# Kernel tuning notes

Measured on AMD Instinct MI355X. Metric: run time of the kernel, lower is better.

Reference implementation:

```python
import jax, jax.numpy as jnp
import numpy as np

N, C_IN, C_RED, H, W = 16, 256, 64, 48, 48


def conv1x1(x, w, b):
    # x: [N, Cin, H, W], w: [Cout, Cin], b: [Cout]
    return jnp.einsum('nchw,oc->nohw', x, w) + b[None, :, None, None]


def setup_inputs() -> dict:
    key = jax.random.key(0)
    ks = jax.random.split(key, 10)
    s_in = 1.0 / np.sqrt(C_IN)
    s_red = 1.0 / np.sqrt(C_RED)
    return {
        'feature_maps': jax.random.normal(ks[0], (N, C_IN, H, W), jnp.float32),
        'global_channel_output': jax.random.normal(ks[1], (N, C_IN, H, W), jnp.float32),
        'Wq': jax.random.uniform(ks[2], (C_RED, C_IN), jnp.float32, -s_in, s_in),
        'bq': jax.random.uniform(ks[3], (C_RED,), jnp.float32, -s_in, s_in),
        'Wk': jax.random.uniform(ks[4], (C_RED, C_IN), jnp.float32, -s_in, s_in),
        'bk': jax.random.uniform(ks[5], (C_RED,), jnp.float32, -s_in, s_in),
        'Wv': jax.random.uniform(ks[6], (C_RED, C_IN), jnp.float32, -s_in, s_in),
        'bv': jax.random.uniform(ks[7], (C_RED,), jnp.float32, -s_in, s_in),
        'Watt': jax.random.uniform(ks[8], (C_IN, C_RED), jnp.float32, -s_red, s_red),
        'batt': jax.random.uniform(ks[9], (C_IN,), jnp.float32, -s_red, s_red),
    }


def reference(feature_maps, global_channel_output, Wq, bq, Wk, bk, Wv, bv, Watt, batt):
    n, _, h, w = feature_maps.shape
    hw = h * w
    q = conv1x1(feature_maps, Wq, bq).reshape(n, -1, hw)   # [N, Cr, HW]
    k = conv1x1(feature_maps, Wk, bk).reshape(n, -1, hw)   # [N, Cr, HW]
    v = conv1x1(feature_maps, Wv, bv).reshape(n, -1, hw)   # [N, Cr, HW]
    # key^T @ query -> [N, HW, HW]
    qk = jnp.einsum('nci,ncj->nij', k, q)
    # global (flattened) softmax over the whole HWxHW matrix per batch element
    qk = jax.nn.softmax(qk.reshape(n, hw * hw), axis=-1).reshape(n, hw, hw)
    att = jnp.einsum('nci,nij->ncj', v, qk).reshape(n, -1, h, w)  # [N, Cr, H, W]
    att = conv1x1(att, Watt, batt)                                 # [N, Cin, H, W]
    return global_channel_output * att + global_channel_output
```

## Files before the change

kernel.cpp:

```cpp
#include <hip/hip_runtime.h>
#include <hip/hip_bf16.h>
#include <stdint.h>

#define NB   16
#define CIN  256
#define CRED 64
#define HW   2304
#define NJT_OUT 36
#define JT_ATT  128
#define NJT_ATT 18
#define NIG  4
#define NIT  9

typedef __bf16 bf16;
typedef __bf16 bf16x8 __attribute__((ext_vector_type(8)));
typedef __bf16 bf16x4 __attribute__((ext_vector_type(4)));
typedef float  f32x4  __attribute__((ext_vector_type(4)));

__global__ __launch_bounds__(256) void prep_kernel(
    const float* __restrict__ Wq, const float* __restrict__ bq,
    const float* __restrict__ Wk, const float* __restrict__ Wv,
    const float* __restrict__ Watt,
    bf16* __restrict__ Wqb, bf16* __restrict__ Wkb, bf16* __restrict__ Wvb,
    bf16* __restrict__ Wab, float* __restrict__ bqs)
{
    const float INVLN2 = 1.44269504088896f;
    int i = blockIdx.x * 256 + threadIdx.x;
    Wqb[i] = (bf16)(Wq[i] * INVLN2);
    Wkb[i] = (bf16)Wk[i];
    Wvb[i] = (bf16)Wv[i];
    Wab[i] = (bf16)Watt[i];
    if (i < CRED) bqs[i] = bq[i] * INVLN2;
}

__global__ __launch_bounds__(256) void qkv_kernel(
    const float* __restrict__ x,
    const bf16* __restrict__ Wqb, const float* __restrict__ bqs,
    const bf16* __restrict__ Wkb, const float* __restrict__ bk,
    const bf16* __restrict__ Wvb, const float* __restrict__ bv,
    bf16* __restrict__ qT, bf16* __restrict__ kT, bf16* __restrict__ v)
{
    __shared__ __align__(16) bf16 sX[32 * 264];
    const int jt = blockIdx.x, n = blockIdx.y;
    const int jbase = jt * 32;
    const int tid = threadIdx.x;
    const int lane = tid & 63, w = tid >> 6;
    const int l15 = lane & 15, q4 = lane >> 4;

    const float* xn = x + ((size_t)n * CIN) * HW + jbase;
    #pragma unroll
    for (int it = 0; it < 8; ++it) {
        int idx = tid + 256 * it;
        int c = idx >> 3, p4 = idx & 7;
        const float4 vv = *(const float4*)(xn + c * HW + p4 * 4);
        sX[(p4 * 4 + 0) * 264 + c] = (bf16)vv.x;
        sX[(p4 * 4 + 1) * 264 + c] = (bf16)vv.y;
        sX[(p4 * 4 + 2) * 264 + c] = (bf16)vv.z;
        sX[(p4 * 4 + 3) * 264 + c] = (bf16)vv.w;
    }
    __syncthreads();

    const bf16*  Ws[3] = {Wqb, Wkb, Wvb};
    const float* bs[3] = {bqs, bk, bv};
    #pragma unroll
    for (int wi = 0; wi < 3; ++wi) {
        bf16x8 a[8];
        const bf16* Wp = Ws[wi] + (w * 16 + l15) * CIN + q4 * 8;
        #pragma unroll
        for (int ks = 0; ks < 8; ++ks) a[ks] = *(const bf16x8*)(Wp + ks * 32);
        f32x4 acc[2] = {};
        #pragma unroll
        for (int nt = 0; nt < 2; ++nt) {
            #pragma unroll
            for (int ks = 0; ks < 8; ++ks) {
                bf16x8 b = *(const bf16x8*)(sX + (nt * 16 + l15) * 264 + ks * 32 + q4 * 8);
                acc[nt] = __builtin_amdgcn_mfma_f32_16x16x32_bf16(a[ks], b, acc[nt], 0, 0, 0);
            }
        }
        const int crb = w * 16 + q4 * 4;
        const float b0 = bs[wi][crb], b1 = bs[wi][crb + 1],
                    b2 = bs[wi][crb + 2], b3 = bs[wi][crb + 3];
        if (wi < 2) {
            bf16* dst = (wi == 0 ? qT : kT) + ((size_t)n * HW) * 64;
            #pragma unroll
            for (int nt = 0; nt < 2; ++nt) {
                int pos = jbase + nt * 16 + l15;
                bf16x4 pk = {(bf16)(acc[nt].x + b0), (bf16)(acc[nt].y + b1),
                             (bf16)(acc[nt].z + b2), (bf16)(acc[nt].w + b3)};
                *(bf16x4*)(dst + pos * 64 + crb) = pk;
            }
        } else {
            bf16* dst = v + ((size_t)n * CRED) * HW;
            #pragma unroll
            for (int nt = 0; nt < 2; ++nt) {
                int pos = jbase + nt * 16 + l15;
                dst[(crb + 0) * HW + pos] = (bf16)(acc[nt].x + b0);
                dst[(crb + 1) * HW + pos] = (bf16)(acc[nt].y + b1);
                dst[(crb + 2) * HW + pos] = (bf16)(acc[nt].z + b2);
                dst[(crb + 3) * HW + pos] = (bf16)(acc[nt].w + b3);
            }
        }
    }
}

__global__ __launch_bounds__(256, 4) void attn_kernel(
    const bf16* __restrict__ qT, const bf16* __restrict__ kT,
    const bf16* __restrict__ v,
    float* __restrict__ OTp, float* __restrict__ Z)
{
    __shared__ __align__(16) bf16 sK[64 * 72];
    __shared__ __align__(16) bf16 sV[64 * 72];
    __shared__ __align__(16) bf16 sP[128 * 72];
    const int jt = blockIdx.x, ig = blockIdx.y, n = blockIdx.z;
    const int jbase = jt * JT_ATT;
    const int tid = threadIdx.x;
    const int lane = tid & 63, w = tid >> 6;
    const int l15 = lane & 15, q4 = lane >> 4;

    bf16x8 qf[2][2];
    {
        const bf16* qn = qT + ((size_t)n * HW + jbase + w * 32) * 64;
        #pragma unroll
        for (int nt = 0; nt < 2; ++nt)
            #pragma unroll
            for (int ks = 0; ks < 2; ++ks)
                qf[nt][ks] = *(const bf16x8*)(qn + (nt * 16 + l15) * 64 + ks * 32 + q4 * 8);
    }

    f32x4 oacc[4][2] = {};
    float zacc = 0.f;
    const uint4* ksrc = (const uint4*)(kT + ((size_t)n * HW) * 64);
    const bf16* vbase = v + ((size_t)n * CRED) * HW;

    const int r0 = tid >> 3, c0 = tid & 7;
    const int ibase0 = ig * NIT * 64;

    uint4 kr0 = ksrc[(ibase0 + r0) * 8 + c0];
    uint4 kr1 = ksrc[(ibase0 + r0 + 32) * 8 + c0];
    uint4 vr0 = *(const uint4*)(vbase + (size_t)r0 * HW + ibase0 + c0 * 8);
    uint4 vr1 = *(const uint4*)(vbase + (size_t)(r0 + 32) * HW + ibase0 + c0 * 8);

    uint4* dk = (uint4*)sK;
    uint4* dv = (uint4*)sV;
    bf16* sPw = sP + (w * 32) * 72;

    for (int it = 0; it < NIT; ++it) {
        __syncthreads();
        dk[r0 * 9 + c0] = kr0;
        dk[(r0 + 32) * 9 + c0] = kr1;
        dv[r0 * 9 + c0] = vr0;
        dv[(r0 + 32) * 9 + c0] = vr1;
        const int nbase = ibase0 + ((it + 1 < NIT) ? (it + 1) * 64 : 0);
        kr0 = ksrc[(nbase + r0) * 8 + c0];
        kr1 = ksrc[(nbase + r0 + 32) * 8 + c0];
        vr0 = *(const uint4*)(vbase + (size_t)r0 * HW + nbase + c0 * 8);
        vr1 = *(const uint4*)(vbase + (size_t)(r0 + 32) * HW + nbase + c0 * 8);
        __syncthreads();

        #pragma unroll
        for (int is = 0; is < 4; ++is) {
            bf16x8 kf0 = *(const bf16x8*)(sK + (is * 16 + l15) * 72 + q4 * 8);
            bf16x8 kf1 = *(const bf16x8*)(sK + (is * 16 + l15) * 72 + 32 + q4 * 8);
            #pragma unroll
            for (int nt = 0; nt < 2; ++nt) {
                f32x4 accs = {};
                accs = __builtin_amdgcn_mfma_f32_16x16x32_bf16(kf0, qf[nt][0], accs, 0, 0, 0);
                accs = __builtin_amdgcn_mfma_f32_16x16x32_bf16(kf1, qf[nt][1], accs, 0, 0, 0);
                float p0 = exp2f(accs.x), p1 = exp2f(accs.y);
                float p2 = exp2f(accs.z), p3 = exp2f(accs.w);
                zacc += (p0 + p1) + (p2 + p3);
                bf16x4 pk = {(bf16)p0, (bf16)p1, (bf16)p2, (bf16)p3};
                *(bf16x4*)(sPw + (nt * 16 + l15) * 72 + is * 16 + q4 * 4) = pk;
            }
        }
        bf16x8 pb[2][2];
        #pragma unroll
        for (int nt = 0; nt < 2; ++nt) {
            pb[nt][0] = *(const bf16x8*)(sPw + (nt * 16 + l15) * 72 + q4 * 8);
            pb[nt][1] = *(const bf16x8*)(sPw + (nt * 16 + l15) * 72 + 32 + q4 * 8);
        }
        #pragma unroll
        for (int ct = 0; ct < 4; ++ct) {
            bf16x8 vf0 = *(const bf16x8*)(sV + (ct * 16 + l15) * 72 + q4 * 8);
            bf16x8 vf1 = *(const bf16x8*)(sV + (ct * 16 + l15) * 72 + 32 + q4 * 8);
            #pragma unroll
            for (int nt = 0; nt < 2; ++nt) {
                oacc[ct][nt] = __builtin_amdgcn_mfma_f32_16x16x32_bf16(vf0, pb[nt][0], oacc[ct][nt], 0, 0, 0);
                oacc[ct][nt] = __builtin_amdgcn_mfma_f32_16x16x32_bf16(vf1, pb[nt][1], oacc[ct][nt], 0, 0, 0);
            }
        }
    }
    float* OTn = OTp + (((size_t)ig * NB + n) * HW) * 64;
    #pragma unroll
    for (int ct = 0; ct < 4; ++ct)
        #pragma unroll
        for (int nt = 0; nt < 2; ++nt) {
            int pos = jbase + w * 32 + nt * 16 + l15;
            *(f32x4*)(OTn + (size_t)pos * 64 + ct * 16 + q4 * 4) = oacc[ct][nt];
        }
    #pragma unroll
    for (int off = 32; off > 0; off >>= 1) zacc += __shfl_down(zacc, off);
    if (lane == 0) atomicAdd(Z + n, zacc);
}

__global__ __launch_bounds__(256) void out_kernel(
    const float* __restrict__ OTp, const float* __restrict__ Z,
    const bf16* __restrict__ Wab, const float* __restrict__ batt,
    const float* __restrict__ g, float* __restrict__ out)
{
    __shared__ __align__(16) bf16 sO[64 * 72];
    const int jt = blockIdx.x, n = blockIdx.y;
    const int jbase = jt * 64;
    const int tid = threadIdx.x;
    const int lane = tid & 63, w = tid >> 6;
    const int l15 = lane & 15, q4 = lane >> 4;
    const float invZ = 1.0f / Z[n];

    for (int i = tid; i < 1024; i += 256) {
        int r = i >> 4, c4 = i & 15;
        const float* p = OTp + (((size_t)n * HW) + jbase + r) * 64 + c4 * 4;
        float4 s = *(const float4*)(p);
        #pragma unroll
        for (int igx = 1; igx < NIG; ++igx) {
            float4 t = *(const float4*)(p + (size_t)igx * NB * HW * 64);
            s.x += t.x; s.y += t.y; s.z += t.z; s.w += t.w;
        }
        bf16x4 pk = {(bf16)(s.x * invZ), (bf16)(s.y * invZ),
                     (bf16)(s.z * invZ), (bf16)(s.w * invZ)};
        *(bf16x4*)(sO + r * 72 + c4 * 4) = pk;
    }
    __syncthreads();

    bf16x8 bfr[4][2];
    #pragma unroll
    for (int nt = 0; nt < 4; ++nt)
        #pragma unroll
        for (int ks = 0; ks < 2; ++ks)
            bfr[nt][ks] = *(const bf16x8*)(sO + (nt * 16 + l15) * 72 + ks * 32 + q4 * 8);

    const float* gp = g + ((size_t)n * CIN) * HW;
    float* op = out + ((size_t)n * CIN) * HW;
    #pragma unroll
    for (int mt = 0; mt < 4; ++mt) {
        const bf16* Wp = Wab + (w * 64 + mt * 16 + l15) * 64 + q4 * 8;
        bf16x8 a0 = *(const bf16x8*)(Wp);
        bf16x8 a1 = *(const bf16x8*)(Wp + 32);
        const int co = w * 64 + mt * 16 + q4 * 4;
        const float c0 = batt[co], c1 = batt[co + 1], c2 = batt[co + 2], c3 = batt[co + 3];
        #pragma unroll
        for (int nt = 0; nt < 4; ++nt) {
            f32x4 acc = {};
            acc = __builtin_amdgcn_mfma_f32_16x16x32_bf16(a0, bfr[nt][0], acc, 0, 0, 0);
            acc = __builtin_amdgcn_mfma_f32_16x16x32_bf16(a1, bfr[nt][1], acc, 0, 0, 0);
            const int pos = jbase + nt * 16 + l15;
            const float g0 = gp[(co + 0) * HW + pos], g1 = gp[(co + 1) * HW + pos];
            const float g2 = gp[(co + 2) * HW + pos], g3 = gp[(co + 3) * HW + pos];
            op[(co + 0) * HW + pos] = g0 * (acc.x + c0 + 1.0f);
            op[(co + 1) * HW + pos] = g1 * (acc.y + c1 + 1.0f);
            op[(co + 2) * HW + pos] = g2 * (acc.z + c2 + 1.0f);
            op[(co + 3) * HW + pos] = g3 * (acc.w + c3 + 1.0f);
        }
    }
}

extern "C" void kernel_launch(void* const* d_in, const int* in_sizes, int n_in,
                              void* d_out, int out_size, void* d_ws, size_t ws_size,
                              hipStream_t stream) {
    const float* x    = (const float*)d_in[0];
    const float* g    = (const float*)d_in[1];
    const float* Wq   = (const float*)d_in[2];
    const float* bq   = (const float*)d_in[3];
    const float* Wk   = (const float*)d_in[4];
    const float* bk   = (const float*)d_in[5];
    const float* Wv   = (const float*)d_in[6];
    const float* bv   = (const float*)d_in[7];
    const float* Watt = (const float*)d_in[8];
    const float* batt = (const float*)d_in[9];
    float* out = (float*)d_out;

    char* ws = (char*)d_ws;
    const size_t qkv_sz = (size_t)NB * HW * CRED * sizeof(bf16);
    bf16*  qT  = (bf16*)(ws);
    bf16*  kT  = (bf16*)(ws + qkv_sz);
    bf16*  vv  = (bf16*)(ws + 2 * qkv_sz);
    float* OTp = (float*)(ws + 3 * qkv_sz);
    char*  w2  = ws + 3 * qkv_sz + (size_t)NIG * NB * HW * CRED * sizeof(float);
    float* Zp  = (float*)(w2);
    bf16*  Wqb = (bf16*)(w2 + 256);
    bf16*  Wkb = Wqb + CRED * CIN;
    bf16*  Wvb = Wkb + CRED * CIN;
    bf16*  Wab = Wvb + CRED * CIN;
    float* bqs = (float*)(Wab + CIN * CRED);

    hipMemsetAsync(Zp, 0, NB * sizeof(float), stream);

    dim3 blk(256);
    prep_kernel<<<dim3(64), blk, 0, stream>>>(Wq, bq, Wk, Wv, Watt, Wqb, Wkb, Wvb, Wab, bqs);
    qkv_kernel<<<dim3(HW / 32, NB), blk, 0, stream>>>(x, Wqb, bqs, Wkb, bk, Wvb, bv, qT, kT, vv);
    attn_kernel<<<dim3(NJT_ATT, NIG, NB), blk, 0, stream>>>(qT, kT, vv, OTp, Zp);
    out_kernel<<<dim3(NJT_OUT, NB), blk, 0, stream>>>(OTp, Zp, Wab, batt, g, out);
}
```

Measured before the change: 248.7 us.

## Keep P in registers, split x transpose into own kernel, shrink out tiles

Several changes land together. The attention kernel no longer round-trips the softmax probabilities through shared memory; they are packed to bf16 with v_cvt_pk_bf16_f32, and a lane shuffle (xor 32) lines up the MFMA B-operand, with the V tile stored in shared memory in a permuted order to match. The QKV projection is split into a separate transpose-to-bf16 kernel, whose output reuses the OTp workspace, and an MFMA kernel that reads the transposed x directly from global memory and computes all three projections in one K loop. The output kernel tile is halved to 32 positions to launch more blocks. The extra launch and extra global traffic for xT add cost, and the permuted V layout adds correctness risk.

```diff
diff --git a/kernel.cpp b/kernel.cpp
--- a/kernel.cpp
+++ b/kernel.cpp
@@ -6,7 +6,6 @@
 #define CIN  256
 #define CRED 64
 #define HW   2304
-#define NJT_OUT 36
 #define JT_ATT  128
 #define NJT_ATT 18
 #define NIG  4
@@ -15,6 +14,7 @@
 typedef __bf16 bf16;
 typedef __bf16 bf16x8 __attribute__((ext_vector_type(8)));
 typedef __bf16 bf16x4 __attribute__((ext_vector_type(4)));
+typedef __bf16 bf16x2 __attribute__((ext_vector_type(2)));
 typedef float  f32x4  __attribute__((ext_vector_type(4)));
 
 __global__ __launch_bounds__(256) void prep_kernel(
@@ -33,72 +33,102 @@
     if (i < CRED) bqs[i] = bq[i] * INVLN2;
 }
 
-__global__ __launch_bounds__(256) void qkv_kernel(
-    const float* __restrict__ x,
+__global__ __launch_bounds__(256) void xpose_kernel(
+    const float* __restrict__ x, bf16* __restrict__ xT)
+{
+    __shared__ bf16 sT[64 * 74];
+    const int pt = blockIdx.x, ct = blockIdx.y, n = blockIdx.z;
+    const int tid = threadIdx.x;
+    const float* xb = x + ((size_t)n * CIN + ct * 64) * HW + pt * 64;
+    #pragma unroll
+    for (int i = 0; i < 4; ++i) {
+        int idx = tid + 256 * i;
+        int c = idx >> 4, p4 = idx & 15;
+        float4 vv = *(const float4*)(xb + (size_t)c * HW + p4 * 4);
+        bf16x2 e0 = {(bf16)vv.x, (bf16)vv.y};
+        bf16x2 e1 = {(bf16)vv.z, (bf16)vv.w};
+        *(bf16x2*)(sT + c * 74 + p4 * 4)     = e0;
+        *(bf16x2*)(sT + c * 74 + p4 * 4 + 2) = e1;
+    }
+    __syncthreads();
+    bf16* xo = xT + ((size_t)n * HW + pt * 64) * 256 + ct * 64;
+    #pragma unroll
+    for (int i = 0; i < 2; ++i) {
+        int idx = tid + 256 * i;
+        int pos = idx >> 3, c8 = (idx & 7) * 8;
+        bf16x8 o;
+        #pragma unroll
+        for (int e = 0; e < 8; ++e) o[e] = sT[(c8 + e) * 74 + pos];
+        *(bf16x8*)(xo + (size_t)pos * 256 + c8) = o;
+    }
+}
+
+__global__ __launch_bounds__(256) void qkvc_kernel(
+    const bf16* __restrict__ xT,
     const bf16* __restrict__ Wqb, const float* __restrict__ bqs,
     const bf16* __restrict__ Wkb, const float* __restrict__ bk,
     const bf16* __restrict__ Wvb, const float* __restrict__ bv,
     bf16* __restrict__ qT, bf16* __restrict__ kT, bf16* __restrict__ v)
 {
-    __shared__ __align__(16) bf16 sX[32 * 264];
     const int jt = blockIdx.x, n = blockIdx.y;
     const int jbase = jt * 32;
     const int tid = threadIdx.x;
     const int lane = tid & 63, w = tid >> 6;
     const int l15 = lane & 15, q4 = lane >> 4;
 
-    const float* xn = x + ((size_t)n * CIN) * HW + jbase;
-    #pragma unroll
-    for (int it = 0; it < 8; ++it) {
-        int idx = tid + 256 * it;
-        int c = idx >> 3, p4 = idx & 7;
-        const float4 vv = *(const float4*)(xn + c * HW + p4 * 4);
-        sX[(p4 * 4 + 0) * 264 + c] = (bf16)vv.x;
-        sX[(p4 * 4 + 1) * 264 + c] = (bf16)vv.y;
-        sX[(p4 * 4 + 2) * 264 + c] = (bf16)vv.z;
-        sX[(p4 * 4 + 3) * 264 + c] = (bf16)vv.w;
-    }
-    __syncthreads();
-
-    const bf16*  Ws[3] = {Wqb, Wkb, Wvb};
-    const float* bs[3] = {bqs, bk, bv};
-    #pragma unroll
-    for (int wi = 0; wi < 3; ++wi) {
-        bf16x8 a[8];
-        const bf16* Wp = Ws[wi] + (w * 16 + l15) * CIN + q4 * 8;
-        #pragma unroll
-        for (int ks = 0; ks < 8; ++ks) a[ks] = *(const bf16x8*)(Wp + ks * 32);
-        f32x4 acc[2] = {};
-        #pragma unroll
-        for (int nt = 0; nt < 2; ++nt) {
-            #pragma unroll
-            for (int ks = 0; ks < 8; ++ks) {
-                bf16x8 b = *(const bf16x8*)(sX + (nt * 16 + l15) * 264 + ks * 32 + q4 * 8);
-                acc[nt] = __builtin_amdgcn_mfma_f32_16x16x32_bf16(a[ks], b, acc[nt], 0, 0, 0);
-            }
-        }
-        const int crb = w * 16 + q4 * 4;
-        const float b0 = bs[wi][crb], b1 = bs[wi][crb + 1],
-                    b2 = bs[wi][crb + 2], b3 = bs[wi][crb + 3];
-        if (wi < 2) {
-            bf16* dst = (wi == 0 ? qT : kT) + ((size_t)n * HW) * 64;
-            #pragma unroll
-            for (int nt = 0; nt < 2; ++nt) {
-                int pos = jbase + nt * 16 + l15;
-                bf16x4 pk = {(bf16)(acc[nt].x + b0), (bf16)(acc[nt].y + b1),
-                             (bf16)(acc[nt].z + b2), (bf16)(acc[nt].w + b3)};
-                *(bf16x4*)(dst + pos * 64 + crb) = pk;
-            }
-        } else {
-            bf16* dst = v + ((size_t)n * CRED) * HW;
-            #pragma unroll
-            for (int nt = 0; nt < 2; ++nt) {
-                int pos = jbase + nt * 16 + l15;
-                dst[(crb + 0) * HW + pos] = (bf16)(acc[nt].x + b0);
-                dst[(crb + 1) * HW + pos] = (bf16)(acc[nt].y + b1);
-                dst[(crb + 2) * HW + pos] = (bf16)(acc[nt].z + b2);
-                dst[(crb + 3) * HW + pos] = (bf16)(acc[nt].w + b3);
-            }
+    const bf16* xb = xT + ((size_t)n * HW + jbase) * 256 + q4 * 8;
+    const bf16* W0 = Wqb + (size_t)(w * 16 + l15) * CIN + q4 * 8;
+    const bf16* W1 = Wkb + (size_t)(w * 16 + l15) * CIN + q4 * 8;
+    const bf16* W2 = Wvb + (size_t)(w * 16 + l15) * CIN + q4 * 8;
+
+    f32x4 acc[3][2] = {};
+    #pragma unroll
+    for (int ks = 0; ks < 8; ++ks) {
+        bf16x8 b0 = *(const bf16x8*)(xb + (size_t)l15 * 256 + ks * 32);
+        bf16x8 b1 = *(const bf16x8*)(xb + (size_t)(16 + l15) * 256 + ks * 32);
+        bf16x8 aq = *(const bf16x8*)(W0 + ks * 32);
+        bf16x8 ak = *(const bf16x8*)(W1 + ks * 32);
+        bf16x8 av = *(const bf16x8*)(W2 + ks * 32);
+        acc[0][0] = __builtin_amdgcn_mfma_f32_16x16x32_bf16(aq, b0, acc[0][0], 0, 0, 0);
+        acc[0][1] = __builtin_amdgcn_mfma_f32_16x16x32_bf16(aq, b1, acc[0][1], 0, 0, 0);
+        acc[1][0] = __builtin_amdgcn_mfma_f32_16x16x32_bf16(ak, b0, acc[1][0], 0, 0, 0);
+        acc[1][1] = __builtin_amdgcn_mfma_f32_16x16x32_bf16(ak, b1, acc[1][1], 0, 0, 0);
+        acc[2][0] = __builtin_amdgcn_mfma_f32_16x16x32_bf16(av, b0, acc[2][0], 0, 0, 0);
+        acc[2][1] = __builtin_amdgcn_mfma_f32_16x16x32_bf16(av, b1, acc[2][1], 0, 0, 0);
+    }
+    const int crb = w * 16 + q4 * 4;
+    {
+        const float b0 = bqs[crb], b1 = bqs[crb+1], b2 = bqs[crb+2], b3 = bqs[crb+3];
+        bf16* dst = qT + ((size_t)n * HW) * 64;
+        #pragma unroll
+        for (int nt = 0; nt < 2; ++nt) {
+            int pos = jbase + nt * 16 + l15;
+            bf16x4 pk = {(bf16)(acc[0][nt].x + b0), (bf16)(acc[0][nt].y + b1),
+                         (bf16)(acc[0][nt].z + b2), (bf16)(acc[0][nt].w + b3)};
+            *(bf16x4*)(dst + (size_t)pos * 64 + crb) = pk;
+        }
+    }
+    {
+        const float b0 = bk[crb], b1 = bk[crb+1], b2 = bk[crb+2], b3 = bk[crb+3];
+        bf16* dst = kT + ((size_t)n * HW) * 64;
+        #pragma unroll
+        for (int nt = 0; nt < 2; ++nt) {
+            int pos = jbase + nt * 16 + l15;
+            bf16x4 pk = {(bf16)(acc[1][nt].x + b0), (bf16)(acc[1][nt].y + b1),
+                         (bf16)(acc[1][nt].z + b2), (bf16)(acc[1][nt].w + b3)};
+            *(bf16x4*)(dst + (size_t)pos * 64 + crb) = pk;
+        }
+    }
+    {
+        const float b0 = bv[crb], b1 = bv[crb+1], b2 = bv[crb+2], b3 = bv[crb+3];
+        bf16* dst = v + ((size_t)n * CRED) * HW;
+        #pragma unroll
+        for (int nt = 0; nt < 2; ++nt) {
+            int pos = jbase + nt * 16 + l15;
+            dst[(crb + 0) * HW + pos] = (bf16)(acc[2][nt].x + b0);
+            dst[(crb + 1) * HW + pos] = (bf16)(acc[2][nt].y + b1);
+            dst[(crb + 2) * HW + pos] = (bf16)(acc[2][nt].z + b2);
+            dst[(crb + 3) * HW + pos] = (bf16)(acc[2][nt].w + b3);
         }
     }
 }
@@ -110,7 +140,6 @@
 {
     __shared__ __align__(16) bf16 sK[64 * 72];
     __shared__ __align__(16) bf16 sV[64 * 72];
-    __shared__ __align__(16) bf16 sP[128 * 72];
     const int jt = blockIdx.x, ig = blockIdx.y, n = blockIdx.z;
     const int jbase = jt * JT_ATT;
     const int tid = threadIdx.x;
@@ -135,58 +164,74 @@
     const int r0 = tid >> 3, c0 = tid & 7;
     const int ibase0 = ig * NIT * 64;
 
+    const int gg = c0 >> 2, m = c0 & 3;
+    const int kbA = ((m >> 1) & 1) | (((m ^ (m >> 1)) & 1) << 2);
+    bf16* vdst0 = sV + r0 * 72 + gg * 32 + kbA * 4;
+    bf16* vdst1 = sV + (r0 + 32) * 72 + gg * 32 + kbA * 4;
+
     uint4 kr0 = ksrc[(ibase0 + r0) * 8 + c0];
     uint4 kr1 = ksrc[(ibase0 + r0 + 32) * 8 + c0];
     uint4 vr0 = *(const uint4*)(vbase + (size_t)r0 * HW + ibase0 + c0 * 8);
     uint4 vr1 = *(const uint4*)(vbase + (size_t)(r0 + 32) * HW + ibase0 + c0 * 8);
 
     uint4* dk = (uint4*)sK;
-    uint4* dv = (uint4*)sV;
-    bf16* sPw = sP + (w * 32) * 72;
 
     for (int it = 0; it < NIT; ++it) {
         __syncthreads();
         dk[r0 * 9 + c0] = kr0;
         dk[(r0 + 32) * 9 + c0] = kr1;
-        dv[r0 * 9 + c0] = vr0;
-        dv[(r0 + 32) * 9 + c0] = vr1;
-        const int nbase = ibase0 + ((it + 1 < NIT) ? (it + 1) * 64 : 0);
+        {
+            uint2 lo, hi;
+            lo.x = vr0.x; lo.y = vr0.y; hi.x = vr0.z; hi.y = vr0.w;
+            *(uint2*)(vdst0) = lo; *(uint2*)(vdst0 + 8) = hi;
+            lo.x = vr1.x; lo.y = vr1.y; hi.x = vr1.z; hi.y = vr1.w;
+            *(uint2*)(vdst1) = lo; *(uint2*)(vdst1 + 8) = hi;
+        }
+        const int ibase = ibase0 + it * 64;
+        const int nbase = (it + 1 < NIT) ? ibase + 64 : ibase0;
         kr0 = ksrc[(nbase + r0) * 8 + c0];
         kr1 = ksrc[(nbase + r0 + 32) * 8 + c0];
         vr0 = *(const uint4*)(vbase + (size_t)r0 * HW + nbase + c0 * 8);
         vr1 = *(const uint4*)(vbase + (size_t)(r0 + 32) * HW + nbase + c0 * 8);
         __syncthreads();
 
+        unsigned pw[2][4][2];
         #pragma unroll
         for (int is = 0; is < 4; ++is) {
             bf16x8 kf0 = *(const bf16x8*)(sK + (is * 16 + l15) * 72 + q4 * 8);
             bf16x8 kf1 = *(const bf16x8*)(sK + (is * 16 + l15) * 72 + 32 + q4 * 8);
             #pragma unroll
             for (int nt = 0; nt < 2; ++nt) {
-                f32x4 accs = {};
-                accs = __builtin_amdgcn_mfma_f32_16x16x32_bf16(kf0, qf[nt][0], accs, 0, 0, 0);
-                accs = __builtin_amdgcn_mfma_f32_16x16x32_bf16(kf1, qf[nt][1], accs, 0, 0, 0);
-                float p0 = exp2f(accs.x), p1 = exp2f(accs.y);
-                float p2 = exp2f(accs.z), p3 = exp2f(accs.w);
+                f32x4 s = {};
+                s = __builtin_amdgcn_mfma_f32_16x16x32_bf16(kf0, qf[nt][0], s, 0, 0, 0);
+                s = __builtin_amdgcn_mfma_f32_16x16x32_bf16(kf1, qf[nt][1], s, 0, 0, 0);
+                float p0 = exp2f(s.x), p1 = exp2f(s.y);
+                float p2 = exp2f(s.z), p3 = exp2f(s.w);
                 zacc += (p0 + p1) + (p2 + p3);
-                bf16x4 pk = {(bf16)p0, (bf16)p1, (bf16)p2, (bf16)p3};
-                *(bf16x4*)(sPw + (nt * 16 + l15) * 72 + is * 16 + q4 * 4) = pk;
+                unsigned w0, w1;
+                asm("v_cvt_pk_bf16_f32 %0, %1, %2" : "=v"(w0) : "v"(p0), "v"(p1));
+                asm("v_cvt_pk_bf16_f32 %0, %1, %2" : "=v"(w1) : "v"(p2), "v"(p3));
+                pw[nt][is][0] = w0;
+                pw[nt][is][1] = w1;
             }
         }
-        bf16x8 pb[2][2];
-        #pragma unroll
-        for (int nt = 0; nt < 2; ++nt) {
-            pb[nt][0] = *(const bf16x8*)(sPw + (nt * 16 + l15) * 72 + q4 * 8);
-            pb[nt][1] = *(const bf16x8*)(sPw + (nt * 16 + l15) * 72 + 32 + q4 * 8);
-        }
-        #pragma unroll
-        for (int ct = 0; ct < 4; ++ct) {
-            bf16x8 vf0 = *(const bf16x8*)(sV + (ct * 16 + l15) * 72 + q4 * 8);
-            bf16x8 vf1 = *(const bf16x8*)(sV + (ct * 16 + l15) * 72 + 32 + q4 * 8);
+        #pragma unroll
+        for (int g = 0; g < 2; ++g) {
+            bf16x8 vf[4];
+            #pragma unroll
+            for (int ct = 0; ct < 4; ++ct)
+                vf[ct] = *(const bf16x8*)(sV + (ct * 16 + l15) * 72 + g * 32 + q4 * 8);
             #pragma unroll
             for (int nt = 0; nt < 2; ++nt) {
-                oacc[ct][nt] = __builtin_amdgcn_mfma_f32_16x16x32_bf16(vf0, pb[nt][0], oacc[ct][nt], 0, 0, 0);
-                oacc[ct][nt] = __builtin_amdgcn_mfma_f32_16x16x32_bf16(vf1, pb[nt][1], oacc[ct][nt], 0, 0, 0);
+                union { unsigned u[4]; bf16x8 v8; } pb;
+                pb.u[0] = pw[nt][2 * g][0];
+                pb.u[1] = pw[nt][2 * g][1];
+                pb.u[2] = (unsigned)__shfl_xor((int)pw[nt][2 * g + 1][0], 32, 64);
+                pb.u[3] = (unsigned)__shfl_xor((int)pw[nt][2 * g + 1][1], 32, 64);
+                #pragma unroll
+                for (int ct = 0; ct < 4; ++ct)
+                    oacc[ct][nt] = __builtin_amdgcn_mfma_f32_16x16x32_bf16(
+                        vf[ct], pb.v8, oacc[ct][nt], 0, 0, 0);
             }
         }
     }
@@ -208,15 +253,17 @@
     const bf16* __restrict__ Wab, const float* __restrict__ batt,
     const float* __restrict__ g, float* __restrict__ out)
 {
-    __shared__ __align__(16) bf16 sO[64 * 72];
+    __shared__ __align__(16) bf16 sO[32 * 72];
     const int jt = blockIdx.x, n = blockIdx.y;
-    const int jbase = jt * 64;
+    const int jbase = jt * 32;
     const int tid = threadIdx.x;
     const int lane = tid & 63, w = tid >> 6;
     const int l15 = lane & 15, q4 = lane >> 4;
     const float invZ = 1.0f / Z[n];
 
-    for (int i = tid; i < 1024; i += 256) {
+    #pragma unroll
+    for (int i0 = 0; i0 < 2; ++i0) {
+        int i = tid + i0 * 256;
         int r = i >> 4, c4 = i & 15;
         const float* p = OTp + (((size_t)n * HW) + jbase + r) * 64 + c4 * 4;
         float4 s = *(const float4*)(p);
@@ -231,9 +278,9 @@
     }
     __syncthreads();
 
-    bf16x8 bfr[4][2];
-    #pragma unroll
-    for (int nt = 0; nt < 4; ++nt)
+    bf16x8 bfr[2][2];
+    #pragma unroll
+    for (int nt = 0; nt < 2; ++nt)
         #pragma unroll
         for (int ks = 0; ks < 2; ++ks)
             bfr[nt][ks] = *(const bf16x8*)(sO + (nt * 16 + l15) * 72 + ks * 32 + q4 * 8);
@@ -248,7 +295,7 @@
         const int co = w * 64 + mt * 16 + q4 * 4;
         const float c0 = batt[co], c1 = batt[co + 1], c2 = batt[co + 2], c3 = batt[co + 3];
         #pragma unroll
-        for (int nt = 0; nt < 4; ++nt) {
+        for (int nt = 0; nt < 2; ++nt) {
             f32x4 acc = {};
             acc = __builtin_amdgcn_mfma_f32_16x16x32_bf16(a0, bfr[nt][0], acc, 0, 0, 0);
             acc = __builtin_amdgcn_mfma_f32_16x16x32_bf16(a1, bfr[nt][1], acc, 0, 0, 0);
@@ -291,12 +338,14 @@
     bf16*  Wvb = Wkb + CRED * CIN;
     bf16*  Wab = Wvb + CRED * CIN;
     float* bqs = (float*)(Wab + CIN * CRED);
+    bf16*  xTb = (bf16*)OTp;
 
     hipMemsetAsync(Zp, 0, NB * sizeof(float), stream);
 
     dim3 blk(256);
     prep_kernel<<<dim3(64), blk, 0, stream>>>(Wq, bq, Wk, Wv, Watt, Wqb, Wkb, Wvb, Wab, bqs);
-    qkv_kernel<<<dim3(HW / 32, NB), blk, 0, stream>>>(x, Wqb, bqs, Wkb, bk, Wvb, bv, qT, kT, vv);
+    xpose_kernel<<<dim3(HW / 64, CIN / 64, NB), blk, 0, stream>>>(x, xTb);
+    qkvc_kernel<<<dim3(HW / 32, NB), blk, 0, stream>>>(xTb, Wqb, bqs, Wkb, bk, Wvb, bv, qT, kT, vv);
     attn_kernel<<<dim3(NJT_ATT, NIG, NB), blk, 0, stream>>>(qT, kT, vv, OTp, Zp);
-    out_kernel<<<dim3(NJT_OUT, NB), blk, 0, stream>>>(OTp, Zp, Wab, batt, g, out);
-}
+    out_kernel<<<dim3(HW / 32, NB), blk, 0, stream>>>(OTp, Zp, Wab, batt, g, out);
+}
```

Result: slower. 258.6 us (+4.0%).
